# Kernel tuning notes

Hardware: AMD Instinct MI355X
Metric: run time of the kernel (lower is better)

Reference implementation:

```python
import jax, jax.numpy as jnp
import numpy as np

Bsz, L, D, N = 2, 2048, 1024, 16
LN_EPS = 1e-5


def setup_inputs() -> dict:
    key = jax.random.key(0)
    ks = jax.random.split(key, 5)
    # A_log initialized as in the module: -log(arange(1, N+1)) broadcast over D
    A_log = -jnp.broadcast_to(jnp.log(jnp.arange(1, N + 1, dtype=jnp.float32))[None, :], (D, N))
    return {
        "x": jax.random.normal(ks[0], (Bsz, L, D), jnp.float32),
        "W_dt": jax.random.normal(ks[1], (D, D), jnp.float32) * 0.02,
        "b_dt": jnp.zeros((D,), jnp.float32),
        "W_B": jax.random.normal(ks[2], (N, D), jnp.float32) * 0.02,
        "W_C": jax.random.normal(ks[3], (N, D), jnp.float32) * 0.02,
        "D_param": jnp.ones((D,), jnp.float32),
        "A_log": A_log,
        "gamma": jnp.ones((D,), jnp.float32),
        "beta": jnp.zeros((D,), jnp.float32),
    }


def reference(x, W_dt, b_dt, W_B, W_C, D_param, A_log, gamma, beta):
    residual = x
    # LayerNorm (biased variance, eps=1e-5)
    mu = jnp.mean(x, axis=-1, keepdims=True)
    var = jnp.var(x, axis=-1, keepdims=True)
    xn = (x - mu) * jax.lax.rsqrt(var + LN_EPS) * gamma + beta

    dt = jax.nn.softplus(xn @ W_dt.T + b_dt)          # (B, L, D)
    A = -jnp.exp(A_log)                                # (D, N)
    B_in = xn @ W_B.T                                  # (B, L, N)
    C_in = xn @ W_C.T                                  # (B, L, N)

    A_bar = jnp.exp(dt[..., None] * A)                 # (B, L, D, N)
    # B_bar[t] * x[t] fused: dt * B_in * xn -> (B, L, D, N)
    Bx = dt[..., None] * B_in[:, :, None, :] * xn[..., None]

    def step(h, inputs):
        a_t, bx_t, c_t = inputs                        # (B,D,N), (B,D,N), (B,N)
        h = a_t * h + bx_t                             # (B, D, N)
        y_t = jnp.einsum('bn,bdn->bd', c_t, h)         # (B, D)
        return h, y_t

    h0 = jnp.zeros((x.shape[0], D, N), x.dtype)
    _, ys = jax.lax.scan(
        step, h0,
        (jnp.transpose(A_bar, (1, 0, 2, 3)),
         jnp.transpose(Bx, (1, 0, 2, 3)),
         jnp.transpose(C_in, (1, 0, 2))))
    y = jnp.transpose(ys, (1, 0, 2)) + D_param * residual
    return y
```

## Files before the change

### kernel.cpp

```cpp
#include <hip/hip_runtime.h>
#include <cstddef>

#define Bsz 2
#define Lr  2048
#define Dr  1024
#define Nr  16
#define M_ROWS (Bsz*Lr)
#define NPAD   1088
#define CHUNK  16
#define NCH    (Lr/CHUNK)

#define BM 64
#define BN 64
#define BK 64
#define NK (Dr/BK)

typedef __attribute__((ext_vector_type(8))) __bf16 bf16x8;
typedef __attribute__((ext_vector_type(4))) float floatx4;

__device__ __forceinline__ unsigned short f2bf(float f) {
    unsigned u = __float_as_uint(f);
    u += 0x7fffu + ((u >> 16) & 1u);
    return (unsigned short)(u >> 16);
}

__device__ __forceinline__ float bf2f(unsigned short u) {
    return __uint_as_float(((unsigned)u) << 16);
}

__device__ __forceinline__ float softplus_f(float x) {
    if (x > 0.f) return x + __logf(1.f + __expf(-x));
    return __logf(1.f + __expf(x));
}

__device__ __forceinline__ void gload_lds16(const unsigned short* g, unsigned short* l) {
    __builtin_amdgcn_global_load_lds((const __attribute__((address_space(1))) void*)g,
                                     (__attribute__((address_space(3))) void*)l, 16, 0, 0);
}

__global__ __launch_bounds__(256) void ln_pack_kernel(const float* __restrict__ x,
                                                      const float* __restrict__ gamma,
                                                      const float* __restrict__ beta,
                                                      unsigned short* __restrict__ xnb,
                                                      const float* __restrict__ Wdt,
                                                      const float* __restrict__ WB,
                                                      const float* __restrict__ WC,
                                                      unsigned short* __restrict__ Wcat) {
    if (blockIdx.x >= M_ROWS) {
        int i = (blockIdx.x - M_ROWS) * 256 + threadIdx.x;
        int row = i >> 10;
        int col = i & 1023;
        float v;
        if (row < Dr)                 v = Wdt[i];
        else if (row < Dr + Nr)       v = WB[(row - Dr) * Dr + col];
        else if (row < Dr + 2*Nr)     v = WC[(row - Dr - Nr) * Dr + col];
        else                          v = 0.f;
        Wcat[i] = f2bf(v);
        return;
    }
    int row = blockIdx.x;
    int tid = threadIdx.x;
    const float4* xr = (const float4*)(x + (size_t)row * Dr);
    float4 v = xr[tid];
    float s  = v.x + v.y + v.z + v.w;
    float ss = v.x*v.x + v.y*v.y + v.z*v.z + v.w*v.w;
    #pragma unroll
    for (int off = 32; off > 0; off >>= 1) {
        s  += __shfl_down(s, off);
        ss += __shfl_down(ss, off);
    }
    __shared__ float red[8];
    int wid = tid >> 6;
    if ((tid & 63) == 0) { red[wid*2] = s; red[wid*2+1] = ss; }
    __syncthreads();
    if (tid == 0) {
        float S = 0.f, SS = 0.f;
        #pragma unroll
        for (int w = 0; w < 4; w++) { S += red[w*2]; SS += red[w*2+1]; }
        float mu  = S * (1.f/Dr);
        float var = SS * (1.f/Dr) - mu*mu;
        red[0] = mu;
        red[1] = rsqrtf(var + 1e-5f);
    }
    __syncthreads();
    float mu = red[0], rs = red[1];
    float4 g = ((const float4*)gamma)[tid], bt = ((const float4*)beta)[tid];
    float4 o;
    o.x = (v.x - mu) * rs * g.x + bt.x;
    o.y = (v.y - mu) * rs * g.y + bt.y;
    o.z = (v.z - mu) * rs * g.z + bt.z;
    o.w = (v.w - mu) * rs * g.w + bt.w;
    ushort4 ob;
    ob.x = f2bf(o.x); ob.y = f2bf(o.y); ob.z = f2bf(o.z); ob.w = f2bf(o.w);
    ((ushort4*)(xnb + (size_t)row * Dr))[tid] = ob;
}

__global__ __launch_bounds__(256) void gemm_kernel(const unsigned short* __restrict__ xnb,
                                                   const unsigned short* __restrict__ w,
                                                   const float* __restrict__ b_dt,
                                                   unsigned short* __restrict__ dt,
                                                   float* __restrict__ bin,
                                                   float* __restrict__ cin) {
    __shared__ unsigned short As[BM * BK];
    __shared__ unsigned short Bs[BN * BK];
    int tid  = threadIdx.x;
    int wave = tid >> 6;
    int lane = tid & 63;
    int lm   = lane & 15;
    int quad = lane >> 4;
    int bid  = blockIdx.x;
    int xcd  = bid & 7;
    int j0   = bid >> 3;
    int nt   = j0 % 17;
    int mt   = (j0 / 17) * 8 + xcd;
    int Mb = mt * BM;
    int Nb = nt * BN;
    int wm = (wave >> 1) * 32;
    int wn = (wave & 1)  * 32;
    int koff = (mt + nt) & (NK - 1);

    int r0 = tid >> 3,         cg0 = (tid & 7) ^ (r0 & 7);
    int r1 = (tid + 256) >> 3, cg1 = ((tid + 256) & 7) ^ (r1 & 7);
    const unsigned short* Ag0 = xnb + (size_t)(Mb + r0) * Dr + cg0 * 8;
    const unsigned short* Ag1 = xnb + (size_t)(Mb + r1) * Dr + cg1 * 8;
    const unsigned short* Bg0 = w   + (size_t)(Nb + r0) * Dr + cg0 * 8;
    const unsigned short* Bg1 = w   + (size_t)(Nb + r1) * Dr + cg1 * 8;
    unsigned short* Al0 = &As[(size_t)tid * 8];
    unsigned short* Al1 = &As[(size_t)(tid + 256) * 8];
    unsigned short* Bl0 = &Bs[(size_t)tid * 8];
    unsigned short* Bl1 = &Bs[(size_t)(tid + 256) * 8];

    floatx4 acc[2][2] = {};

    for (int kk = 0; kk < NK; kk++) {
        int k0 = ((kk + koff) & (NK - 1)) * BK;
        gload_lds16(Ag0 + k0, Al0);
        gload_lds16(Ag1 + k0, Al1);
        gload_lds16(Bg0 + k0, Bl0);
        gload_lds16(Bg1 + k0, Bl1);
        __syncthreads();
        #pragma unroll
        for (int s = 0; s < 2; s++) {
            int ra0 = wm + lm, ra1 = wm + 16 + lm;
            int rb0 = wn + lm, rb1 = wn + 16 + lm;
            int cg = s * 4 + quad;
            bf16x8 a0 = *(const bf16x8*)&As[ra0 * BK + ((cg ^ (ra0 & 7)) * 8)];
            bf16x8 a1 = *(const bf16x8*)&As[ra1 * BK + ((cg ^ (ra1 & 7)) * 8)];
            bf16x8 b0 = *(const bf16x8*)&Bs[rb0 * BK + ((cg ^ (rb0 & 7)) * 8)];
            bf16x8 b1 = *(const bf16x8*)&Bs[rb1 * BK + ((cg ^ (rb1 & 7)) * 8)];
            acc[0][0] = __builtin_amdgcn_mfma_f32_16x16x32_bf16(a0, b0, acc[0][0], 0, 0, 0);
            acc[0][1] = __builtin_amdgcn_mfma_f32_16x16x32_bf16(a0, b1, acc[0][1], 0, 0, 0);
            acc[1][0] = __builtin_amdgcn_mfma_f32_16x16x32_bf16(a1, b0, acc[1][0], 0, 0, 0);
            acc[1][1] = __builtin_amdgcn_mfma_f32_16x16x32_bf16(a1, b1, acc[1][1], 0, 0, 0);
        }
        __syncthreads();
    }

    #pragma unroll
    for (int i = 0; i < 2; i++) {
        int grow0 = Mb + wm + i * 16 + quad * 4;
        #pragma unroll
        for (int jj = 0; jj < 2; jj++) {
            int gcol = Nb + wn + jj * 16 + lm;
            #pragma unroll
            for (int r = 0; r < 4; r++) {
                float v = acc[i][jj][r];
                int row = grow0 + r;
                if (gcol < Dr) {
                    dt[(size_t)row * Dr + gcol] = f2bf(softplus_f(v + b_dt[gcol]));
                } else if (gcol < Dr + Nr) {
                    bin[(size_t)row * Nr + (gcol - Dr)] = v;
                } else if (gcol < Dr + 2*Nr) {
                    cin[(size_t)row * Nr + (gcol - Dr - Nr)] = v;
                }
            }
        }
    }
}

__global__ __launch_bounds__(256) void scan1_kernel(const unsigned short* __restrict__ dtb,
                                                    const unsigned short* __restrict__ xnb,
                                                    const float* __restrict__ bin,
                                                    const float* __restrict__ A_log,
                                                    float* __restrict__ Sws,
                                                    unsigned short* __restrict__ hendws) {
    int tid = threadIdx.x;
    int d  = blockIdx.x * 256 + tid;
    int ch = blockIdx.y;
    int b  = blockIdx.z;
    size_t rowbase = (size_t)b * Lr + ch * CHUNK;

    float ac[16];
    #pragma unroll
    for (int i = 0; i < 4; i++) {
        float4 t = ((const float4*)(A_log + (size_t)d * Nr))[i];
        ac[i*4+0] = -__expf(t.x);
        ac[i*4+1] = -__expf(t.y);
        ac[i*4+2] = -__expf(t.z);
        ac[i*4+3] = -__expf(t.w);
    }

    __shared__ float lb[CHUNK * Nr];
    lb[tid] = bin[rowbase * Nr + tid];
    __syncthreads();

    float dtv[CHUNK], xv[CHUNK];
    {
        const unsigned short* dtp = dtb + rowbase * Dr + d;
        const unsigned short* xp  = xnb + rowbase * Dr + d;
        #pragma unroll
        for (int t = 0; t < CHUNK; t++) {
            dtv[t] = bf2f(dtp[(size_t)t * Dr]);
            xv[t]  = bf2f(xp[(size_t)t * Dr]);
        }
    }

    float h[16];
    #pragma unroll
    for (int n = 0; n < 16; n++) h[n] = 0.f;
    float S = 0.f;

    #pragma unroll
    for (int t = 0; t < CHUNK; t++) {
        float dv = dtv[t];
        S += dv;
        float cm = dv * xv[t];
        const float4* br4 = (const float4*)(lb + t * Nr);
        float4 q0 = br4[0], q1 = br4[1], q2 = br4[2], q3 = br4[3];
        float bb[16] = {q0.x,q0.y,q0.z,q0.w, q1.x,q1.y,q1.z,q1.w,
                        q2.x,q2.y,q2.z,q2.w, q3.x,q3.y,q3.z,q3.w};
        #pragma unroll
        for (int n = 0; n < 16; n++)
            h[n] = __expf(dv * ac[n]) * h[n] + cm * bb[n];
    }

    Sws[(size_t)(b * NCH + ch) * Dr + d] = S;
    size_t obase = ((size_t)(b * NCH + ch) * Nr) * Dr + d;
    #pragma unroll
    for (int n = 0; n < 16; n++)
        hendws[obase + (size_t)n * Dr] = f2bf(h[n]);
}

__global__ __launch_bounds__(256) void combine_kernel(const float* __restrict__ Sws,
                                                      const unsigned short* __restrict__ hendws,
                                                      const float* __restrict__ A_log,
                                                      unsigned short* __restrict__ hinws) {
    int id = blockIdx.x * 256 + threadIdx.x;
    int b  = id >> 14;
    int dn = id & 16383;
    int n  = dn >> 10;
    int d  = dn & 1023;
    float ac = -__expf(A_log[d * Nr + n]);
    size_t sbase = (size_t)b * NCH * Dr + d;
    size_t base  = (size_t)b * NCH * (Nr * Dr) + dn;
    float hin = 0.f;
    for (int cb = 0; cb < NCH; cb += 16) {
        float p16[16], he[16];
        #pragma unroll
        for (int u = 0; u < 16; u++) {
            p16[u] = Sws[sbase + (size_t)(cb + u) * Dr];
            he[u]  = bf2f(hendws[base + (size_t)(cb + u) * (Nr * Dr)]);
        }
        #pragma unroll
        for (int u = 0; u < 16; u++) p16[u] = __expf(p16[u] * ac);
        #pragma unroll
        for (int u = 0; u < 16; u++) {
            size_t idx = base + (size_t)(cb + u) * (Nr * Dr);
            hinws[idx] = f2bf(hin);
            hin = p16[u] * hin + he[u];
        }
    }
}

__global__ __launch_bounds__(256) void scan2_kernel(const unsigned short* __restrict__ dtb,
                                                    const unsigned short* __restrict__ xnb,
                                                    const float* __restrict__ bin,
                                                    const float* __restrict__ cin,
                                                    const float* __restrict__ A_log,
                                                    const unsigned short* __restrict__ hinws,
                                                    const float* __restrict__ x,
                                                    const float* __restrict__ Dp,
                                                    float* __restrict__ out) {
    int tid = threadIdx.x;
    int d  = blockIdx.x * 256 + tid;
    int ch = blockIdx.y;
    int b  = blockIdx.z;
    size_t rowbase = (size_t)b * Lr + ch * CHUNK;

    float ac[16];
    #pragma unroll
    for (int i = 0; i < 4; i++) {
        float4 t = ((const float4*)(A_log + (size_t)d * Nr))[i];
        ac[i*4+0] = -__expf(t.x);
        ac[i*4+1] = -__expf(t.y);
        ac[i*4+2] = -__expf(t.z);
        ac[i*4+3] = -__expf(t.w);
    }

    __shared__ float lb[CHUNK * Nr];
    __shared__ float lc[CHUNK * Nr];
    lb[tid] = bin[rowbase * Nr + tid];
    lc[tid] = cin[rowbase * Nr + tid];
    __syncthreads();

    float dtv[CHUNK], xv[CHUNK];
    {
        const unsigned short* dtp = dtb + rowbase * Dr + d;
        const unsigned short* xp  = xnb + rowbase * Dr + d;
        #pragma unroll
        for (int t = 0; t < CHUNK; t++) {
            dtv[t] = bf2f(dtp[(size_t)t * Dr]);
            xv[t]  = bf2f(xp[(size_t)t * Dr]);
        }
    }

    size_t obase = ((size_t)(b * NCH + ch) * Nr) * Dr + d;
    float h[16];
    #pragma unroll
    for (int n = 0; n < 16; n++) h[n] = bf2f(hinws[obase + (size_t)n * Dr]);

    float dp = Dp[d];
    const float* xr = x   + rowbase * Dr + d;
    float* op       = out + rowbase * Dr + d;

    for (int tb = 0; tb < CHUNK; tb += 4) {
        float xr4[4];
        #pragma unroll
        for (int u = 0; u < 4; u++) xr4[u] = xr[(size_t)(tb + u) * Dr];
        #pragma unroll
        for (int u = 0; u < 4; u++) {
            int t = tb + u;
            float dv = dtv[t];
            float cm = dv * xv[t];
            const float4* br4 = (const float4*)(lb + t * Nr);
            const float4* cr4 = (const float4*)(lc + t * Nr);
            float4 q0 = br4[0], q1 = br4[1], q2 = br4[2], q3 = br4[3];
            float4 r0 = cr4[0], r1 = cr4[1], r2 = cr4[2], r3 = cr4[3];
            float bb[16] = {q0.x,q0.y,q0.z,q0.w, q1.x,q1.y,q1.z,q1.w,
                            q2.x,q2.y,q2.z,q2.w, q3.x,q3.y,q3.z,q3.w};
            float cc[16] = {r0.x,r0.y,r0.z,r0.w, r1.x,r1.y,r1.z,r1.w,
                            r2.x,r2.y,r2.z,r2.w, r3.x,r3.y,r3.z,r3.w};
            float y = 0.f;
            #pragma unroll
            for (int n = 0; n < 16; n++) {
                h[n] = __expf(dv * ac[n]) * h[n] + cm * bb[n];
                y += cc[n] * h[n];
            }
            op[(size_t)t * Dr] = y + dp * xr4[u];
        }
    }
}

extern "C" void kernel_launch(void* const* d_in, const int* in_sizes, int n_in,
                              void* d_out, int out_size, void* d_ws, size_t ws_size,
                              hipStream_t stream) {
    const float* x      = (const float*)d_in[0];
    const float* W_dt   = (const float*)d_in[1];
    const float* b_dt   = (const float*)d_in[2];
    const float* W_B    = (const float*)d_in[3];
    const float* W_C    = (const float*)d_in[4];
    const float* Dparam = (const float*)d_in[5];
    const float* A_log  = (const float*)d_in[6];
    const float* gamma  = (const float*)d_in[7];
    const float* beta   = (const float*)d_in[8];
    float* out = (float*)d_out;

    char* ws = (char*)d_ws;
    unsigned short* xnb  = (unsigned short*)(ws);
    unsigned short* wcat = (unsigned short*)(ws + 8388608);
    unsigned short* dtb  = (unsigned short*)(ws + 10616832);
    float*          bin  = (float*)(ws + 19005440);
    float*          cin  = (float*)(ws + 19267584);
    float*          Sws  = (float*)(ws + 19529728);
    unsigned short* hend = (unsigned short*)(ws + 20578304);
    unsigned short* hin  = (unsigned short*)(ws + 28966912);

    ln_pack_kernel<<<M_ROWS + (NPAD * Dr) / 256, 256, 0, stream>>>(
        x, gamma, beta, xnb, W_dt, W_B, W_C, wcat);
    gemm_kernel<<<(M_ROWS / BM) * (NPAD / BN), 256, 0, stream>>>(xnb, wcat, b_dt, dtb, bin, cin);
    dim3 sgrid(Dr / 256, NCH, Bsz);
    scan1_kernel<<<sgrid, 256, 0, stream>>>(dtb, xnb, bin, A_log, Sws, hend);
    combine_kernel<<<(Bsz * Dr * Nr) / 256, 256, 0, stream>>>(Sws, hend, A_log, hin);
    scan2_kernel<<<sgrid, 256, 0, stream>>>(dtb, xnb, bin, cin, A_log, hin, x, Dparam, out);
}
```

Baseline: 149.8 us.

## Rewrite GEMM as single-wave 64x64 tiles with triple-buffered async LDS prefetch

The projection GEMM now runs one wave per block, and that wave computes the whole 64x64 output tile with a 4x4 grid of MFMA accumulators. The K step shrinks to 32 and LDS is triple-buffered, so global-to-LDS loads are issued two steps ahead with no block barriers. The aim is to remove __syncthreads stalls and to raise MFMA work per LDS read. The cost is fewer waves per CU to hide latency and more accumulator registers. It also relies on the compiler inserting waits for the async LDS loads before they are read.

Measured after the change: 174.9 us. +16.8%, slower.

```diff
diff --git a/kernel.cpp b/kernel.cpp
--- a/kernel.cpp
+++ b/kernel.cpp
@@ -10,10 +10,8 @@
 #define CHUNK  16
 #define NCH    (Lr/CHUNK)
 
-#define BM 64
-#define BN 64
-#define BK 64
-#define NK (Dr/BK)
+#define GBK 32
+#define GNK (Dr/GBK)
 
 typedef __attribute__((ext_vector_type(8))) __bf16 bf16x8;
 typedef __attribute__((ext_vector_type(4))) float floatx4;
@@ -95,73 +93,73 @@
     ((ushort4*)(xnb + (size_t)row * Dr))[tid] = ob;
 }
 
-__global__ __launch_bounds__(256) void gemm_kernel(const unsigned short* __restrict__ xnb,
-                                                   const unsigned short* __restrict__ w,
-                                                   const float* __restrict__ b_dt,
-                                                   unsigned short* __restrict__ dt,
-                                                   float* __restrict__ bin,
-                                                   float* __restrict__ cin) {
-    __shared__ unsigned short As[BM * BK];
-    __shared__ unsigned short Bs[BN * BK];
-    int tid  = threadIdx.x;
-    int wave = tid >> 6;
-    int lane = tid & 63;
-    int lm   = lane & 15;
-    int quad = lane >> 4;
+__global__ __launch_bounds__(64) void gemm_kernel(const unsigned short* __restrict__ xnb,
+                                                  const unsigned short* __restrict__ w,
+                                                  const float* __restrict__ b_dt,
+                                                  unsigned short* __restrict__ dt,
+                                                  float* __restrict__ bin,
+                                                  float* __restrict__ cin) {
+    __shared__ unsigned short As[3][64 * GBK];
+    __shared__ unsigned short Bs[3][64 * GBK];
+    int t    = threadIdx.x;
+    int lm   = t & 15;
+    int quad = t >> 4;
     int bid  = blockIdx.x;
     int xcd  = bid & 7;
-    int j0   = bid >> 3;
-    int nt   = j0 % 17;
-    int mt   = (j0 / 17) * 8 + xcd;
-    int Mb = mt * BM;
-    int Nb = nt * BN;
-    int wm = (wave >> 1) * 32;
-    int wn = (wave & 1)  * 32;
-    int koff = (mt + nt) & (NK - 1);
-
-    int r0 = tid >> 3,         cg0 = (tid & 7) ^ (r0 & 7);
-    int r1 = (tid + 256) >> 3, cg1 = ((tid + 256) & 7) ^ (r1 & 7);
-    const unsigned short* Ag0 = xnb + (size_t)(Mb + r0) * Dr + cg0 * 8;
-    const unsigned short* Ag1 = xnb + (size_t)(Mb + r1) * Dr + cg1 * 8;
-    const unsigned short* Bg0 = w   + (size_t)(Nb + r0) * Dr + cg0 * 8;
-    const unsigned short* Bg1 = w   + (size_t)(Nb + r1) * Dr + cg1 * 8;
-    unsigned short* Al0 = &As[(size_t)tid * 8];
-    unsigned short* Al1 = &As[(size_t)(tid + 256) * 8];
-    unsigned short* Bl0 = &Bs[(size_t)tid * 8];
-    unsigned short* Bl1 = &Bs[(size_t)(tid + 256) * 8];
-
-    floatx4 acc[2][2] = {};
-
-    for (int kk = 0; kk < NK; kk++) {
-        int k0 = ((kk + koff) & (NK - 1)) * BK;
-        gload_lds16(Ag0 + k0, Al0);
-        gload_lds16(Ag1 + k0, Al1);
-        gload_lds16(Bg0 + k0, Bl0);
-        gload_lds16(Bg1 + k0, Bl1);
-        __syncthreads();
-        #pragma unroll
-        for (int s = 0; s < 2; s++) {
-            int ra0 = wm + lm, ra1 = wm + 16 + lm;
-            int rb0 = wn + lm, rb1 = wn + 16 + lm;
-            int cg = s * 4 + quad;
-            bf16x8 a0 = *(const bf16x8*)&As[ra0 * BK + ((cg ^ (ra0 & 7)) * 8)];
-            bf16x8 a1 = *(const bf16x8*)&As[ra1 * BK + ((cg ^ (ra1 & 7)) * 8)];
-            bf16x8 b0 = *(const bf16x8*)&Bs[rb0 * BK + ((cg ^ (rb0 & 7)) * 8)];
-            bf16x8 b1 = *(const bf16x8*)&Bs[rb1 * BK + ((cg ^ (rb1 & 7)) * 8)];
-            acc[0][0] = __builtin_amdgcn_mfma_f32_16x16x32_bf16(a0, b0, acc[0][0], 0, 0, 0);
-            acc[0][1] = __builtin_amdgcn_mfma_f32_16x16x32_bf16(a0, b1, acc[0][1], 0, 0, 0);
-            acc[1][0] = __builtin_amdgcn_mfma_f32_16x16x32_bf16(a1, b0, acc[1][0], 0, 0, 0);
-            acc[1][1] = __builtin_amdgcn_mfma_f32_16x16x32_bf16(a1, b1, acc[1][1], 0, 0, 0);
-        }
-        __syncthreads();
-    }
-
-    #pragma unroll
-    for (int i = 0; i < 2; i++) {
-        int grow0 = Mb + wm + i * 16 + quad * 4;
-        #pragma unroll
-        for (int jj = 0; jj < 2; jj++) {
-            int gcol = Nb + wn + jj * 16 + lm;
+    int j    = bid >> 3;
+    int nt   = j % 17;
+    int mt   = (j / 17) * 8 + xcd;
+    int Mb = mt * 64;
+    int Nb = nt * 64;
+    int koff = (mt + nt) & (GNK - 1);
+
+    int cg = (t & 3) ^ ((t >> 3) & 3);
+    const unsigned short* Ag = xnb + (size_t)(Mb + (t >> 2)) * Dr + cg * 8;
+    const unsigned short* Bg = w   + (size_t)(Nb + (t >> 2)) * Dr + cg * 8;
+
+    #pragma unroll
+    for (int s = 0; s < 2; s++) {
+        int k0 = ((s + koff) & (GNK - 1)) * GBK;
+        #pragma unroll
+        for (int c = 0; c < 4; c++) {
+            gload_lds16(Ag + (size_t)c * 16 * Dr + k0, &As[s][c * 512] + t * 8);
+            gload_lds16(Bg + (size_t)c * 16 * Dr + k0, &Bs[s][c * 512] + t * 8);
+        }
+    }
+
+    floatx4 acc[4][4] = {};
+
+    #pragma unroll
+    for (int kk = 0; kk < GNK; kk++) {
+        int cur = kk % 3;
+        bf16x8 a[4], b[4];
+        #pragma unroll
+        for (int i = 0; i < 4; i++) {
+            int ra = i * 16 + lm;
+            int csa = quad ^ ((ra >> 1) & 3);
+            a[i] = *(const bf16x8*)&As[cur][ra * GBK + csa * 8];
+            b[i] = *(const bf16x8*)&Bs[cur][ra * GBK + csa * 8];
+        }
+        int nb = (kk + 2) % 3;
+        int k2 = ((kk + 2 + koff) & (GNK - 1)) * GBK;
+        #pragma unroll
+        for (int c = 0; c < 4; c++) {
+            gload_lds16(Ag + (size_t)c * 16 * Dr + k2, &As[nb][c * 512] + t * 8);
+            gload_lds16(Bg + (size_t)c * 16 * Dr + k2, &Bs[nb][c * 512] + t * 8);
+        }
+        #pragma unroll
+        for (int i = 0; i < 4; i++)
+            #pragma unroll
+            for (int jj = 0; jj < 4; jj++)
+                acc[i][jj] = __builtin_amdgcn_mfma_f32_16x16x32_bf16(a[i], b[jj], acc[i][jj], 0, 0, 0);
+    }
+
+    #pragma unroll
+    for (int i = 0; i < 4; i++) {
+        int grow0 = Mb + i * 16 + quad * 4;
+        #pragma unroll
+        for (int jj = 0; jj < 4; jj++) {
+            int gcol = Nb + jj * 16 + lm;
             #pragma unroll
             for (int r = 0; r < 4; r++) {
                 float v = acc[i][jj][r];
@@ -377,7 +375,7 @@
 
     ln_pack_kernel<<<M_ROWS + (NPAD * Dr) / 256, 256, 0, stream>>>(
         x, gamma, beta, xnb, W_dt, W_B, W_C, wcat);
-    gemm_kernel<<<(M_ROWS / BM) * (NPAD / BN), 256, 0, stream>>>(xnb, wcat, b_dt, dtb, bin, cin);
+    gemm_kernel<<<(M_ROWS / 64) * (NPAD / 64), 64, 0, stream>>>(xnb, wcat, b_dt, dtb, bin, cin);
     dim3 sgrid(Dr / 256, NCH, Bsz);
     scan1_kernel<<<sgrid, 256, 0, stream>>>(dtb, xnb, bin, A_log, Sws, hend);
     combine_kernel<<<(Bsz * Dr * Nr) / 256, 256, 0, stream>>>(Sws, hend, A_log, hin);
```
